# Kernel tuning notes

Measured on AMD Instinct MI355X. Metric: run time of the kernel, lower is better.

## Reference

```python
import math
import jax, jax.numpy as jnp
import numpy as np

EMBED_DIM = 2048
NUM_HEADS = 16
HEAD_DIM = EMBED_DIM // NUM_HEADS
CHUNK = 128
RMS_EPS = 1e-5


def _build_slopes(n):
    # ALiBi-style slopes (power-of-2 branch; n=16 is a power of 2)
    def pow2(n):
        start = 2.0 ** (-(2.0 ** -(math.log2(n) - 3)))
        return [start * (start ** i) for i in range(n)]
    if math.log2(n).is_integer():
        s = pow2(n)
    else:
        closest = 2 ** math.floor(math.log2(n))
        s = pow2(closest) + pow2(2 * closest)[0::2][: n - closest]
    return jnp.asarray(s, dtype=jnp.float32)


def _rotary(x_BTHD, offset=0):
    # x: [B, T, H, D]; D//4 nonzero freqs + D//4 zero freqs -> D//2 angles
    T, D = x_BTHD.shape[1], x_BTHD.shape[-1]
    freq = (1.0 / 1024.0) ** jnp.linspace(0.0, 1.0, D // 4, dtype=jnp.float32)
    freq = jnp.concatenate([freq, jnp.zeros(D // 4, dtype=jnp.float32)])
    t = jnp.arange(offset, offset + T, dtype=jnp.float32)
    theta = t[:, None] * freq[None, :]            # [T, D/2]
    cos = jnp.cos(theta)[None, :, None, :]
    sin = jnp.sin(theta)[None, :, None, :]
    x1, x2 = jnp.split(x_BTHD.astype(jnp.float32), 2, axis=-1)
    y1 = x1 * cos + x2 * sin
    y2 = -x1 * sin + x2 * cos
    return jnp.concatenate([y1, y2], axis=-1).astype(x_BTHD.dtype)


def _lightning_attn(q, k, v, slopes):
    # q,k,v: [B, H, T, D]; decayed causal linear attention:
    #   o_t = q_t @ sum_{s<=t} exp(-slope*(t-s)) * k_s v_s^T
    B, H, T, D = q.shape
    C = CHUNK
    NC = T // C
    r = jnp.exp(-slopes)                          # [H]
    i = jnp.arange(C, dtype=jnp.float32)
    # factors within a chunk
    q_decay = r[:, None] ** (i[None, :] + 1.0)    # [H, C] : r^{i+1}
    k_decay = r[:, None] ** (C - 1.0 - i[None, :])  # [H, C] : r^{C-1-i}
    diff = i[:, None] - i[None, :]                # t - s
    mask = diff >= 0
    dmask = jnp.where(mask[None], r[:, None, None] ** jnp.where(mask, diff, 0.0)[None], 0.0)  # [H,C,C]
    r_C = r ** float(C)                            # [H]

    def reshape_chunks(x):
        return x.reshape(B, H, NC, C, D).transpose(2, 0, 1, 3, 4)  # [NC,B,H,C,D]

    qc, kc, vc = reshape_chunks(q), reshape_chunks(k), reshape_chunks(v)

    def step(kv, qkv):
        qi, ki, vi = qkv                          # [B,H,C,D]
        inter = jnp.einsum('bhcd,bhde->bhce', qi * q_decay[None, :, :, None], kv)
        scores = jnp.einsum('bhcd,bhsd->bhcs', qi, ki) * dmask[None]
        intra = jnp.einsum('bhcs,bhse->bhce', scores, vi)
        kv_new = r_C[None, :, None, None] * kv + jnp.einsum(
            'bhcd,bhce->bhde', ki * k_decay[None, :, :, None], vi)
        return kv_new, inter + intra

    kv0 = jnp.zeros((B, H, D, D), dtype=q.dtype)
    _, out = jax.lax.scan(step, kv0, (qc, kc, vc))  # [NC,B,H,C,D]
    return out.transpose(1, 2, 0, 3, 4).reshape(B, H, T, D)


def _rms_norm(x, w):
    var = jnp.mean(jnp.square(x), axis=-1, keepdims=True)
    return x * jax.lax.rsqrt(var + RMS_EPS) * w


def setup_inputs() -> dict:
    key = jax.random.key(0)
    ks = jax.random.split(key, 6)
    sc = 1.0 / math.sqrt(EMBED_DIM)
    return {
        'x': jax.random.normal(ks[0], (4, 4096, EMBED_DIM), dtype=jnp.float32),
        'Wq': jax.random.normal(ks[1], (EMBED_DIM, EMBED_DIM), dtype=jnp.float32) * sc,
        'Wk': jax.random.normal(ks[2], (EMBED_DIM, EMBED_DIM), dtype=jnp.float32) * sc,
        'Wv': jax.random.normal(ks[3], (EMBED_DIM, EMBED_DIM), dtype=jnp.float32) * sc,
        'Wo': jax.random.normal(ks[4], (EMBED_DIM, EMBED_DIM), dtype=jnp.float32) * sc,
        'rms_w': jnp.ones((EMBED_DIM,), dtype=jnp.float32),
    }


def reference(x, Wq, Wk, Wv, Wo, rms_w):
    B, T, E = x.shape
    H, D = NUM_HEADS, HEAD_DIM
    q = (x @ Wq).reshape(B, T, H, D)
    k = (x @ Wk).reshape(B, T, H, D)
    v = (x @ Wv).reshape(B, T, H, D)
    q = _rotary(q)
    k = _rotary(k)
    q, k, v = (t.transpose(0, 2, 1, 3) for t in (q, k, v))  # [B,H,T,D]
    slopes = _build_slopes(H)
    attn = _lightning_attn(q, k, v, slopes)       # [B,H,T,D]
    attn = attn.transpose(0, 2, 1, 3).reshape(B, T, E)
    attn = _rms_norm(attn, rms_w)
    return attn @ Wo
```

## Files before the change

kernel.cpp:

```cpp
#include <hip/hip_runtime.h>

typedef unsigned short ushort;
typedef float f32x4 __attribute__((ext_vector_type(4)));
typedef __bf16 bf16x8 __attribute__((ext_vector_type(8)));
typedef ushort u16x4 __attribute__((ext_vector_type(4)));
typedef ushort u16x8 __attribute__((ext_vector_type(8)));

#define LOG2E 1.4426950408889634f

__device__ __forceinline__ ushort f2bu(float f) { __bf16 b = (__bf16)f; return __builtin_bit_cast(ushort, b); }
__device__ __forceinline__ float  bu2f(ushort u) { return (float)__builtin_bit_cast(__bf16, u); }

__device__ __forceinline__ void gld16(const void* g, void* l) {
    __builtin_amdgcn_global_load_lds((const __attribute__((address_space(1))) unsigned int*)g,
                                     (__attribute__((address_space(3))) unsigned int*)l, 16, 0, 0);
}

__global__ __launch_bounds__(256) void k_cvt(const float* __restrict__ in, ushort* __restrict__ out, int n4) {
    int i = blockIdx.x * 256 + threadIdx.x;
    if (i < n4) {
        float4 v = ((const float4*)in)[i];
        u16x4 o = { f2bu(v.x), f2bu(v.y), f2bu(v.z), f2bu(v.w) };
        ((u16x4*)out)[i] = o;
    }
}

__global__ __launch_bounds__(256) void k_twt4(const float* __restrict__ W0, const float* __restrict__ W1,
                                              const float* __restrict__ W2, const float* __restrict__ W3,
                                              ushort* __restrict__ D0, ushort* __restrict__ D1,
                                              ushort* __restrict__ D2, ushort* __restrict__ D3) {
    int z = blockIdx.z;
    const float* W = (z == 0) ? W0 : (z == 1) ? W1 : (z == 2) ? W2 : W3;
    ushort* Wt = (z == 0) ? D0 : (z == 1) ? D1 : (z == 2) ? D2 : D3;
    __shared__ float t[32][33];
    int n0 = blockIdx.x * 32, k0 = blockIdx.y * 32;
    int tx = threadIdx.x & 31, ty = threadIdx.x >> 5;
#pragma unroll
    for (int i = 0; i < 32; i += 8) t[ty + i][tx] = W[(size_t)(k0 + ty + i) * 2048 + n0 + tx];
    __syncthreads();
#pragma unroll
    for (int i = 0; i < 32; i += 8) Wt[(size_t)(n0 + ty + i) * 2048 + k0 + tx] = f2bu(t[tx][ty + i]);
}

__global__ __launch_bounds__(256) void k_rope(float* __restrict__ tab) {
    int idx = blockIdx.x * 256 + threadIdx.x;
    int t = idx >> 5, j = idx & 31;
    float fr = exp2f(-10.0f * (float)j / 31.0f);
    float th = (float)t * fr;
    tab[idx * 2]     = cosf(th);
    tab[idx * 2 + 1] = sinf(th);
}

#define AOFF(buf, kh) ((buf) * 32768 + (kh) * 16384)
#define BOFF(buf, kh) (65536 + (buf) * 32768 + (kh) * 16384)

#define STG_A(BUFX, KHX, KKX) do {                                                 \
    gld16(asrc0 + ((KKX) + (KHX) * 32) * 2, lds + AOFF(BUFX, KHX) + ldst);         \
    gld16(asrc1 + ((KKX) + (KHX) * 32) * 2, lds + AOFF(BUFX, KHX) + 8192 + ldst);  \
} while (0)
#define STG_B(BUFX, KHX, KKX) do {                                                 \
    gld16(bsrc0 + ((KKX) + (KHX) * 32) * 2, lds + BOFF(BUFX, KHX) + ldst);         \
    gld16(bsrc1 + ((KKX) + (KHX) * 32) * 2, lds + BOFF(BUFX, KHX) + 8192 + ldst);  \
} while (0)

#define PHASE(BUF, KH, MH, LDB, STAGE_STMT, TAILVM) do {                           \
    bf16x8 af_[4];                                                                 \
    const char* ab_ = lds + AOFF(BUF, KH);                                         \
    _Pragma("unroll")                                                              \
    for (int mi_ = 0; mi_ < 4; ++mi_)                                              \
        af_[mi_] = *(const bf16x8*)(ab_ + offA[(MH) * 4 + mi_]);                   \
    if (LDB) {                                                                     \
        const char* bb_ = lds + BOFF(BUF, KH);                                     \
        _Pragma("unroll")                                                          \
        for (int ni_ = 0; ni_ < 4; ++ni_)                                          \
            bfr[ni_] = *(const bf16x8*)(bb_ + offB[ni_]);                          \
    }                                                                              \
    STAGE_STMT;                                                                    \
    __builtin_amdgcn_s_barrier();                                                  \
    asm volatile("s_waitcnt lgkmcnt(0)" ::: "memory");                             \
    __builtin_amdgcn_sched_barrier(0);                                             \
    __builtin_amdgcn_s_setprio(1);                                                 \
    _Pragma("unroll")                                                              \
    for (int mi_ = 0; mi_ < 4; ++mi_)                                              \
        _Pragma("unroll")                                                          \
        for (int ni_ = 0; ni_ < 4; ++ni_)                                          \
            acc[(MH) * 4 + mi_][ni_] = __builtin_amdgcn_mfma_f32_16x16x32_bf16(    \
                af_[mi_], bfr[ni_], acc[(MH) * 4 + mi_][ni_], 0, 0, 0);            \
    __builtin_amdgcn_s_setprio(0);                                                 \
    TAILVM;                                                                        \
    __builtin_amdgcn_s_barrier();                                                  \
} while (0)

#define TILE(BUF, TC) do {                                                         \
    int tp1_ = (TC) + 1 < 32 ? (TC) + 1 : 31;                                      \
    int tp2_ = (TC) + 2 < 32 ? (TC) + 2 : 31;                                      \
    int kb1_ = tp1_ * 64, kb2_ = tp2_ * 64;                                        \
    PHASE(BUF, 0, 0, 1, STG_A((BUF) ^ 1, 1, kb1_), ((void)0));                     \
    PHASE(BUF, 0, 1, 0, STG_B((BUF) ^ 1, 1, kb1_),                                 \
          asm volatile("s_waitcnt vmcnt(8)" ::: "memory"));                        \
    PHASE(BUF, 1, 0, 1, STG_A(BUF, 0, kb2_), ((void)0));                           \
    PHASE(BUF, 1, 1, 0, STG_B(BUF, 0, kb2_),                                       \
          asm volatile("s_waitcnt vmcnt(8)" ::: "memory"));                        \
} while (0)

template <int MODE>
__global__ __launch_bounds__(512, 2) void k_gemm(const ushort* __restrict__ A, const ushort* __restrict__ Bt,
                                                 const float* __restrict__ rt, float* __restrict__ Cf,
                                                 ushort* __restrict__ qa, ushort* __restrict__ ka,
                                                 ushort* __restrict__ kTa, ushort* __restrict__ vTa) {
    __shared__ __align__(128) char lds[131072];
    const int tid = threadIdx.x;
    const int wid = tid >> 6, lane = tid & 63;
    const int wm = wid >> 2, wn = wid & 3;
    const int lrow = lane & 15, q = lane >> 4;

    int bid = blockIdx.x;
    int xcd = bid & 7, local = bid >> 3;
    int nt, mloc;
    if (MODE == 0) { nt = xcd + (local % 3) * 8; mloc = local / 3; }
    else           { nt = local & 7;             mloc = xcd * 8 + (local >> 3); }
    const size_t n0 = (size_t)nt * 256;
    const size_t m0 = (size_t)mloc * 256;

    int offA[8], offB[4];
#pragma unroll
    for (int mi = 0; mi < 8; ++mi) {
        int R = wm * 128 + mi * 16 + lrow;
        offA[mi] = R * 64 + ((q ^ ((R >> 1) & 3)) << 4);
    }
#pragma unroll
    for (int ni = 0; ni < 4; ++ni) {
        int R = wn * 64 + ni * 16 + lrow;
        offB[ni] = R * 64 + ((q ^ ((R >> 1) & 3)) << 4);
    }

    int srow0 = tid >> 2;
    int cw = (tid & 3) ^ ((tid >> 3) & 3);
    const char* asrc0 = (const char*)(A + (m0 + srow0) * 2048 + cw * 8);
    const char* asrc1 = (const char*)(A + (m0 + srow0 + 128) * 2048 + cw * 8);
    const char* bsrc0 = (const char*)(Bt + (n0 + srow0) * 2048 + cw * 8);
    const char* bsrc1 = (const char*)(Bt + (n0 + srow0 + 128) * 2048 + cw * 8);
    const int ldst = tid * 16;

    f32x4 acc[8][4] = {};
    bf16x8 bfr[4];

    STG_A(0, 0, 0); STG_B(0, 0, 0); STG_A(0, 1, 0); STG_B(0, 1, 0);
    STG_A(1, 0, 64); STG_B(1, 0, 64);
    asm volatile("s_waitcnt vmcnt(8)" ::: "memory");
    __builtin_amdgcn_s_barrier();

#pragma unroll 1
    for (int t = 0; t < 32; t += 2) {
        TILE(0, t);
        TILE(1, t + 1);
    }

    if (MODE == 1) {
#pragma unroll
        for (int mi = 0; mi < 8; ++mi)
#pragma unroll
            for (int ni = 0; ni < 4; ++ni)
#pragma unroll
                for (int i = 0; i < 4; ++i) {
                    size_t row = m0 + wm * 128 + mi * 16 + q * 4 + i;
                    size_t col = n0 + wn * 64 + ni * 16 + lrow;
                    Cf[row * 2048 + col] = acc[mi][ni][i];
                }
        return;
    }

    asm volatile("s_waitcnt vmcnt(0)" ::: "memory");
    __syncthreads();
    ushort* lt = (ushort*)lds;
    const int tsel = nt >> 3;
    const int b = (int)(m0 >> 12);
    const int t0base = (int)(m0 & 4095);
    const int hbase = (nt & 7) * 2;

    for (int st = 0; st < 2; ++st) {
        if (wm == st) {
#pragma unroll
            for (int mi = 0; mi < 8; ++mi)
#pragma unroll
                for (int ni = 0; ni < 4; ++ni)
#pragma unroll
                    for (int i = 0; i < 4; ++i)
                        lt[(mi * 16 + q * 4 + i) * 258 + wn * 64 + ni * 16 + lrow] = f2bu(acc[mi][ni][i]);
        }
        __syncthreads();
        const int t0 = t0base + st * 128;
        if (tsel != 2) {
            int cid = tid & 31, rquad = tid >> 5;
            int d0 = cid * 4;
            ushort* dstN = (tsel == 0 ? qa : ka);
#pragma unroll 2
            for (int it = 0; it < 16; ++it) {
                int hl = it >> 3, rr = (it & 7) * 16 + rquad;
                int t = t0 + rr;
                const ushort* src = &lt[rr * 258 + hl * 128];
                ushort o[4];
                if (d0 < 32) {
#pragma unroll
                    for (int j = 0; j < 4; ++j) {
                        int d = d0 + j;
                        float2 cssn = *(const float2*)&rt[(t * 32 + d) * 2];
                        float x1 = bu2f(src[d]), x2 = bu2f(src[d + 64]);
                        o[j] = f2bu(x1 * cssn.x + x2 * cssn.y);
                    }
                } else if (d0 >= 64 && d0 < 96) {
#pragma unroll
                    for (int j = 0; j < 4; ++j) {
                        int d = d0 + j;
                        float2 cssn = *(const float2*)&rt[(t * 32 + (d - 64)) * 2];
                        float x1 = bu2f(src[d - 64]), x2 = bu2f(src[d]);
                        o[j] = f2bu(x2 * cssn.x - x1 * cssn.y);
                    }
                } else {
#pragma unroll
                    for (int j = 0; j < 4; ++j) o[j] = src[d0 + j];
                }
                int bh = b * 16 + hbase + hl;
                u16x4 ov = { o[0], o[1], o[2], o[3] };
                *(u16x4*)(dstN + ((size_t)bh * 4096 + t) * 128 + d0) = ov;
                if (tsel == 1 && (d0 < 32 || (d0 >= 64 && d0 < 96))) {
                    ushort* wb = &lt[rr * 258 + hl * 128 + d0];
                    wb[0] = o[0]; wb[1] = o[1]; wb[2] = o[2]; wb[3] = o[3];
                }
            }
        }
        if (tsel != 0) {
            __syncthreads();
            int sb = tid & 31, dgrp = tid >> 5;
            int s0 = sb * 4;
            ushort* dstT = (tsel == 1 ? kTa : vTa);
#pragma unroll 2
            for (int it = 0; it < 16; ++it) {
                int hl = it >> 3, dd = (it & 7) * 16 + dgrp;
                int bh = b * 16 + hbase + hl;
                float l2r_h = -exp2f(-0.5f * (float)(hbase + hl + 1)) * LOG2E;
                ushort o[4];
#pragma unroll
                for (int j = 0; j < 4; ++j) {
                    int s = s0 + j;
                    float v = bu2f(lt[s * 258 + hl * 128 + dd]);
                    if (tsel == 1) v *= exp2f(l2r_h * (float)(127 - s));
                    o[j] = f2bu(v);
                }
                u16x4 ov = { o[0], o[1], o[2], o[3] };
                *(u16x4*)(dstT + ((size_t)bh * 128 + dd) * 4096 + t0 + s0) = ov;
            }
        }
        __syncthreads();
    }
}

__global__ __launch_bounds__(256) void k_pass1(const ushort* __restrict__ kTa, const ushort* __restrict__ vTa,
                                               float* __restrict__ KVlo, float* __restrict__ KVhi) {
    int blk = blockIdx.x;
    int c = blk & 31, bh = blk >> 5;
    __shared__ __align__(16) ushort lv[128][136];
    __shared__ __align__(16) ushort lk[128][136];
    int tid = threadIdx.x;
#pragma unroll
    for (int i = 0; i < 8; ++i) {
        int idx = i * 256 + tid; int row = idx >> 4, cb = (idx & 15) * 8;
        *(bf16x8*)&lv[row][cb] = *(const bf16x8*)(vTa + ((size_t)bh * 128 + row) * 4096 + c * 128 + cb);
        *(bf16x8*)&lk[row][cb] = *(const bf16x8*)(kTa + ((size_t)bh * 128 + row) * 4096 + c * 128 + cb);
    }
    __syncthreads();
    int wid = tid >> 6, lane = tid & 63, wr = wid >> 1, wc = wid & 1;
    int lrow = lane & 15, lko = (lane >> 4) * 8;
    f32x4 acc[4][4] = {};
#pragma unroll
    for (int ks = 0; ks < 4; ++ks) {
        bf16x8 a[4], bb[4];
#pragma unroll
        for (int mi = 0; mi < 4; ++mi) a[mi] = *(const bf16x8*)&lv[wr * 64 + mi * 16 + lrow][ks * 32 + lko];
#pragma unroll
        for (int ni = 0; ni < 4; ++ni) bb[ni] = *(const bf16x8*)&lk[wc * 64 + ni * 16 + lrow][ks * 32 + lko];
#pragma unroll
        for (int mi = 0; mi < 4; ++mi)
#pragma unroll
            for (int ni = 0; ni < 4; ++ni)
                acc[mi][ni] = __builtin_amdgcn_mfma_f32_16x16x32_bf16(a[mi], bb[ni], acc[mi][ni], 0, 0, 0);
    }
    float* out = (bh < 32) ? (KVlo + (size_t)blk * 16384) : (KVhi + (size_t)(blk - 1024) * 16384);
#pragma unroll
    for (int mi = 0; mi < 4; ++mi)
#pragma unroll
        for (int ni = 0; ni < 4; ++ni)
#pragma unroll
            for (int i = 0; i < 4; ++i)
                out[(wr * 64 + mi * 16 + (lane >> 4) * 4 + i) * 128 + wc * 64 + ni * 16 + lrow] = acc[mi][ni][i];
}

__global__ __launch_bounds__(256) void k_scan(const float* __restrict__ KVlo, const float* __restrict__ KVhi,
                                              ushort* __restrict__ KVbf) {
    int bh = blockIdx.x >> 4, seg = blockIdx.x & 15, h = bh & 15;
    float slope = exp2f(-0.5f * (float)(h + 1));
    float rC = exp2f(-slope * LOG2E * 128.0f);
    int off = seg * 1024 + threadIdx.x * 4;
    const float* base = (bh < 32) ? (KVlo + (size_t)bh * 32 * 16384) : (KVhi + (size_t)(bh - 32) * 32 * 16384);
    f32x4 st = {0.f, 0.f, 0.f, 0.f};
    for (int c = 0; c < 32; ++c) {
        f32x4 v = *(const f32x4*)(base + (size_t)c * 16384 + off);
        u16x4 o = { f2bu(st.x), f2bu(st.y), f2bu(st.z), f2bu(st.w) };
        *(u16x4*)(KVbf + ((size_t)bh * 32 + c) * 16384 + off) = o;
        st = st * rC + v;
    }
}

__global__ __launch_bounds__(512) void k_pass3(const ushort* __restrict__ qa, const ushort* __restrict__ ka,
                                               const ushort* __restrict__ vTa, const ushort* __restrict__ KVbf,
                                               ushort* __restrict__ attn) {
    int blk = blockIdx.x;
    int c = blk & 31, bh = blk >> 5, h = bh & 15;
    __shared__ __align__(16) ushort lq[128][136];
    __shared__ __align__(16) ushort lk[128][136];
    __shared__ __align__(16) ushort lv[128][136];
    int tid = threadIdx.x;
#pragma unroll
    for (int i = 0; i < 4; ++i) {
        int idx = i * 512 + tid; int row = idx >> 4, cb = (idx & 15) * 8;
        *(bf16x8*)&lq[row][cb] = *(const bf16x8*)(qa + ((size_t)bh * 4096 + c * 128 + row) * 128 + cb);
        *(bf16x8*)&lk[row][cb] = *(const bf16x8*)(ka + ((size_t)bh * 4096 + c * 128 + row) * 128 + cb);
        *(bf16x8*)&lv[row][cb] = *(const bf16x8*)(vTa + ((size_t)bh * 128 + row) * 4096 + c * 128 + cb);
    }
    __syncthreads();
    int wid = tid >> 6, lane = tid & 63;
    int wr = wid >> 2, wc = wid & 3;
    int lrow = lane & 15, lko = (lane >> 4) * 8;
    float slope = exp2f(-0.5f * (float)(h + 1));
    float l2r = -slope * LOG2E;

    f32x4 accs[4][2] = {};
#pragma unroll
    for (int kd = 0; kd < 4; ++kd) {
        bf16x8 a[4], bb[2];
#pragma unroll
        for (int mi = 0; mi < 4; ++mi) a[mi] = *(const bf16x8*)&lq[wr * 64 + mi * 16 + lrow][kd * 32 + lko];
#pragma unroll
        for (int ni = 0; ni < 2; ++ni) bb[ni] = *(const bf16x8*)&lk[wc * 32 + ni * 16 + lrow][kd * 32 + lko];
#pragma unroll
        for (int mi = 0; mi < 4; ++mi)
#pragma unroll
            for (int ni = 0; ni < 2; ++ni)
                accs[mi][ni] = __builtin_amdgcn_mfma_f32_16x16x32_bf16(a[mi], bb[ni], accs[mi][ni], 0, 0, 0);
    }
    __syncthreads();

    f32x4 acc[4][2] = {};
#pragma unroll
    for (int kd = 0; kd < 4; ++kd) {
        bf16x8 a[4], bb[2];
#pragma unroll
        for (int mi = 0; mi < 4; ++mi) a[mi] = *(const bf16x8*)&lq[wr * 64 + mi * 16 + lrow][kd * 32 + lko];
#pragma unroll
        for (int ni = 0; ni < 2; ++ni)
            bb[ni] = *(const bf16x8*)(KVbf + (size_t)blk * 16384 + (size_t)(wc * 32 + ni * 16 + lrow) * 128 + kd * 32 + lko);
#pragma unroll
        for (int mi = 0; mi < 4; ++mi)
#pragma unroll
            for (int ni = 0; ni < 2; ++ni)
                acc[mi][ni] = __builtin_amdgcn_mfma_f32_16x16x32_bf16(a[mi], bb[ni], acc[mi][ni], 0, 0, 0);
    }

#pragma unroll
    for (int mi = 0; mi < 4; ++mi)
#pragma unroll
        for (int ni = 0; ni < 2; ++ni)
#pragma unroll
            for (int i = 0; i < 4; ++i) {
                int t = wr * 64 + mi * 16 + (lane >> 4) * 4 + i;
                int s = wc * 32 + ni * 16 + lrow;
                int dt = t - s;
                float w = (dt < 0) ? 0.f : exp2f(l2r * (float)dt);
                lk[t][s] = f2bu(accs[mi][ni][i] * w);
            }

#pragma unroll
    for (int mi = 0; mi < 4; ++mi)
#pragma unroll
        for (int ni = 0; ni < 2; ++ni)
#pragma unroll
            for (int i = 0; i < 4; ++i) {
                int t = wr * 64 + mi * 16 + (lane >> 4) * 4 + i;
                acc[mi][ni][i] *= exp2f(l2r * (float)(t + 1));
            }
    __syncthreads();

#pragma unroll
    for (int ks = 0; ks < 4; ++ks) {
        bf16x8 a[4], bb[2];
#pragma unroll
        for (int mi = 0; mi < 4; ++mi) a[mi] = *(const bf16x8*)&lk[wr * 64 + mi * 16 + lrow][ks * 32 + lko];
#pragma unroll
        for (int ni = 0; ni < 2; ++ni) bb[ni] = *(const bf16x8*)&lv[wc * 32 + ni * 16 + lrow][ks * 32 + lko];
#pragma unroll
        for (int mi = 0; mi < 4; ++mi)
#pragma unroll
            for (int ni = 0; ni < 2; ++ni)
                acc[mi][ni] = __builtin_amdgcn_mfma_f32_16x16x32_bf16(a[mi], bb[ni], acc[mi][ni], 0, 0, 0);
    }

    ushort* out = attn + ((size_t)bh * 4096 + c * 128) * 128;
#pragma unroll
    for (int mi = 0; mi < 4; ++mi)
#pragma unroll
        for (int ni = 0; ni < 2; ++ni)
#pragma unroll
            for (int i = 0; i < 4; ++i)
                out[(size_t)(wr * 64 + mi * 16 + (lane >> 4) * 4 + i) * 128 + wc * 32 + ni * 16 + lrow] =
                    f2bu(acc[mi][ni][i]);
}

__global__ __launch_bounds__(256) void k_rms(const ushort* __restrict__ attn, const float* __restrict__ w,
                                             ushort* __restrict__ normed) {
    int tok = blockIdx.x; int b = tok >> 12, t = tok & 4095;
    int tid = threadIdx.x;
    int e0 = tid * 8; int h = e0 >> 7, d0 = e0 & 127;
    bf16x8 v = *(const bf16x8*)(attn + (((size_t)(b * 16 + h) * 4096 + t) * 128 + d0));
    float f[8]; float ss = 0.f;
#pragma unroll
    for (int j = 0; j < 8; ++j) { f[j] = (float)v[j]; ss += f[j] * f[j]; }
#pragma unroll
    for (int o = 1; o < 64; o <<= 1) ss += __shfl_xor(ss, o, 64);
    __shared__ float red[4];
    if ((tid & 63) == 0) red[tid >> 6] = ss;
    __syncthreads();
    float tot = red[0] + red[1] + red[2] + red[3];
    float sc = rsqrtf(tot * (1.0f / 2048.0f) + 1e-5f);
    u16x8 ov;
#pragma unroll
    for (int j = 0; j < 8; ++j) ov[j] = f2bu(f[j] * sc * w[e0 + j]);
    *(u16x8*)(normed + (size_t)tok * 2048 + e0) = ov;
}

extern "C" void kernel_launch(void* const* d_in, const int* in_sizes, int n_in,
                              void* d_out, int out_size, void* d_ws, size_t ws_size,
                              hipStream_t stream) {
    const float* x    = (const float*)d_in[0];
    const float* Wq   = (const float*)d_in[1];
    const float* Wk   = (const float*)d_in[2];
    const float* Wv   = (const float*)d_in[3];
    const float* Wo   = (const float*)d_in[4];
    const float* rmsw = (const float*)d_in[5];
    char* ws = (char*)d_ws;
    const size_t MiB = 1ull << 20;
    ushort* WtQKV = (ushort*)(ws + 0);
    ushort* WtK   = (ushort*)(ws + 8 * MiB);
    ushort* WtV   = (ushort*)(ws + 16 * MiB);
    ushort* WtO   = (ushort*)(ws + 24 * MiB);
    ushort* xb    = (ushort*)(ws + 32 * MiB);
    ushort* qa    = (ushort*)(ws + 96 * MiB);
    ushort* ka    = (ushort*)(ws + 160 * MiB);
    ushort* kTa   = (ushort*)(ws + 224 * MiB);
    ushort* vTa   = (ushort*)(ws + 288 * MiB);
    float*  rt    = (float*)(ws + 352 * MiB);
    float*  KVlo  = (float*)(ws + 32 * MiB);
    float*  KVhi  = (float*)(ws + 353 * MiB);
    ushort* KVbf  = (ushort*)(ws + 224 * MiB);
    ushort* attn  = (ushort*)(ws + 32 * MiB);
    ushort* nrm   = (ushort*)(ws + 96 * MiB);

    k_cvt<<<32768, 256, 0, stream>>>(x, xb, 8388608);
    dim3 gw(64, 64, 4);
    k_twt4<<<gw, 256, 0, stream>>>(Wq, Wk, Wv, Wo, WtQKV, WtK, WtV, WtO);
    k_rope<<<512, 256, 0, stream>>>(rt);

    k_gemm<0><<<1536, 512, 0, stream>>>(xb, WtQKV, rt, nullptr, qa, ka, kTa, vTa);

    k_pass1<<<2048, 256, 0, stream>>>(kTa, vTa, KVlo, KVhi);
    k_scan<<<1024, 256, 0, stream>>>(KVlo, KVhi, KVbf);
    k_pass3<<<2048, 512, 0, stream>>>(qa, ka, vTa, KVbf, attn);

    k_rms<<<16384, 256, 0, stream>>>(attn, rmsw, nrm);
    k_gemm<1><<<512, 512, 0, stream>>>(nrm, WtO, nullptr, (float*)d_out, nullptr, nullptr, nullptr, nullptr);
}
```

Before: 822.2 us.

## Transpose GEMM epilogue LDS tile and store per-chunk KV states in bf16

The QKV GEMM epilogue now stages its tile in LDS column-major (d-major, pitch 130) with packed 32-bit writes. The rope and transposed-store passes restructure their thread mapping around this layout, writing pairs of elements at a time. Per-chunk KV outer products from pass1 are now stored as bf16 in one contiguous buffer instead of fp32 split across two regions, which halves pass1 write and scan read traffic. The cost is lower precision for the chunk states fed into the scan, and the rope path's LDS reads are now strided, so bank conflicts may change.

```diff
diff --git a/kernel.cpp b/kernel.cpp
--- a/kernel.cpp
+++ b/kernel.cpp
@@ -1,6 +1,7 @@
 #include <hip/hip_runtime.h>
 
 typedef unsigned short ushort;
+typedef unsigned int uint;
 typedef float f32x4 __attribute__((ext_vector_type(4)));
 typedef __bf16 bf16x8 __attribute__((ext_vector_type(8)));
 typedef ushort u16x4 __attribute__((ext_vector_type(4)));
@@ -10,6 +11,7 @@
 
 __device__ __forceinline__ ushort f2bu(float f) { __bf16 b = (__bf16)f; return __builtin_bit_cast(ushort, b); }
 __device__ __forceinline__ float  bu2f(ushort u) { return (float)__builtin_bit_cast(__bf16, u); }
+__device__ __forceinline__ uint   pk2(float a, float b) { return (uint)f2bu(a) | ((uint)f2bu(b) << 16); }
 
 __device__ __forceinline__ void gld16(const void* g, void* l) {
     __builtin_amdgcn_global_load_lds((const __attribute__((address_space(1))) unsigned int*)g,
@@ -183,49 +185,51 @@
 #pragma unroll
             for (int mi = 0; mi < 8; ++mi)
 #pragma unroll
-                for (int ni = 0; ni < 4; ++ni)
-#pragma unroll
-                    for (int i = 0; i < 4; ++i)
-                        lt[(mi * 16 + q * 4 + i) * 258 + wn * 64 + ni * 16 + lrow] = f2bu(acc[mi][ni][i]);
+                for (int ni = 0; ni < 4; ++ni) {
+                    int col = wn * 64 + ni * 16 + lrow;
+                    int r0 = mi * 16 + q * 4;
+                    uint* p = (uint*)&lt[col * 130 + r0];
+                    p[0] = pk2(acc[mi][ni][0], acc[mi][ni][1]);
+                    p[1] = pk2(acc[mi][ni][2], acc[mi][ni][3]);
+                }
         }
         __syncthreads();
         const int t0 = t0base + st * 128;
+
         if (tsel != 2) {
-            int cid = tid & 31, rquad = tid >> 5;
-            int d0 = cid * 4;
+            int cid = tid & 63, rgrp = tid >> 6;
             ushort* dstN = (tsel == 0 ? qa : ka);
 #pragma unroll 2
-            for (int it = 0; it < 16; ++it) {
-                int hl = it >> 3, rr = (it & 7) * 16 + rquad;
-                int t = t0 + rr;
-                const ushort* src = &lt[rr * 258 + hl * 128];
-                ushort o[4];
-                if (d0 < 32) {
-#pragma unroll
-                    for (int j = 0; j < 4; ++j) {
-                        int d = d0 + j;
-                        float2 cssn = *(const float2*)&rt[(t * 32 + d) * 2];
-                        float x1 = bu2f(src[d]), x2 = bu2f(src[d + 64]);
-                        o[j] = f2bu(x1 * cssn.x + x2 * cssn.y);
+            for (int hl = 0; hl < 2; ++hl) {
+                int bh = b * 16 + hbase + hl;
+                size_t rowbase = ((size_t)bh * 4096 + t0) * 128;
+#pragma unroll 4
+                for (int it = 0; it < 16; ++it) {
+                    int rr = it * 8 + rgrp;
+                    int t = t0 + rr;
+                    if (cid < 16) {
+                        int d0 = cid * 2;
+                        float4 cs = *(const float4*)&rt[(t * 32 + d0) * 2];
+                        float xa0 = bu2f(lt[(hl * 128 + d0) * 130 + rr]);
+                        float xa1 = bu2f(lt[(hl * 128 + d0 + 1) * 130 + rr]);
+                        float xb0 = bu2f(lt[(hl * 128 + d0 + 64) * 130 + rr]);
+                        float xb1 = bu2f(lt[(hl * 128 + d0 + 65) * 130 + rr]);
+                        uint y1 = pk2(xa0 * cs.x + xb0 * cs.y, xa1 * cs.z + xb1 * cs.w);
+                        uint y2 = pk2(xb0 * cs.x - xa0 * cs.y, xb1 * cs.z - xa1 * cs.w);
+                        *(uint*)(dstN + rowbase + (size_t)rr * 128 + d0) = y1;
+                        *(uint*)(dstN + rowbase + (size_t)rr * 128 + d0 + 64) = y2;
+                        if (tsel == 1) {
+                            lt[(hl * 128 + d0) * 130 + rr] = (ushort)(y1 & 0xffff);
+                            lt[(hl * 128 + d0 + 1) * 130 + rr] = (ushort)(y1 >> 16);
+                            lt[(hl * 128 + d0 + 64) * 130 + rr] = (ushort)(y2 & 0xffff);
+                            lt[(hl * 128 + d0 + 65) * 130 + rr] = (ushort)(y2 >> 16);
+                        }
+                    } else if (cid < 48) {
+                        int d0 = (cid < 32) ? (2 * cid) : (32 + 2 * cid);
+                        uint v = (uint)lt[(hl * 128 + d0) * 130 + rr] |
+                                 ((uint)lt[(hl * 128 + d0 + 1) * 130 + rr] << 16);
+                        *(uint*)(dstN + rowbase + (size_t)rr * 128 + d0) = v;
                     }
-                } else if (d0 >= 64 && d0 < 96) {
-#pragma unroll
-                    for (int j = 0; j < 4; ++j) {
-                        int d = d0 + j;
-                        float2 cssn = *(const float2*)&rt[(t * 32 + (d - 64)) * 2];
-                        float x1 = bu2f(src[d - 64]), x2 = bu2f(src[d]);
-                        o[j] = f2bu(x2 * cssn.x - x1 * cssn.y);
-                    }
-                } else {
-#pragma unroll
-                    for (int j = 0; j < 4; ++j) o[j] = src[d0 + j];
-                }
-                int bh = b * 16 + hbase + hl;
-                u16x4 ov = { o[0], o[1], o[2], o[3] };
-                *(u16x4*)(dstN + ((size_t)bh * 4096 + t) * 128 + d0) = ov;
-                if (tsel == 1 && (d0 < 32 || (d0 >= 64 && d0 < 96))) {
-                    ushort* wb = &lt[rr * 258 + hl * 128 + d0];
-                    wb[0] = o[0]; wb[1] = o[1]; wb[2] = o[2]; wb[3] = o[3];
                 }
             }
         }
@@ -234,21 +238,27 @@
             int sb = tid & 31, dgrp = tid >> 5;
             int s0 = sb * 4;
             ushort* dstT = (tsel == 1 ? kTa : vTa);
-#pragma unroll 2
-            for (int it = 0; it < 16; ++it) {
-                int hl = it >> 3, dd = (it & 7) * 16 + dgrp;
+            for (int hl = 0; hl < 2; ++hl) {
                 int bh = b * 16 + hbase + hl;
                 float l2r_h = -exp2f(-0.5f * (float)(hbase + hl + 1)) * LOG2E;
-                ushort o[4];
-#pragma unroll
-                for (int j = 0; j < 4; ++j) {
-                    int s = s0 + j;
-                    float v = bu2f(lt[s * 258 + hl * 128 + dd]);
-                    if (tsel == 1) v *= exp2f(l2r_h * (float)(127 - s));
-                    o[j] = f2bu(v);
+#pragma unroll 2
+                for (int itg = 0; itg < 8; ++itg) {
+                    int dd = itg * 16 + dgrp;
+                    const uint* p = (const uint*)&lt[(hl * 128 + dd) * 130 + s0];
+                    uint w0 = p[0], w1 = p[1];
+                    u16x4 ov;
+                    if (tsel == 1) {
+                        float v0 = bu2f((ushort)(w0 & 0xffff)) * exp2f(l2r_h * (float)(127 - s0));
+                        float v1 = bu2f((ushort)(w0 >> 16))    * exp2f(l2r_h * (float)(126 - s0));
+                        float v2 = bu2f((ushort)(w1 & 0xffff)) * exp2f(l2r_h * (float)(125 - s0));
+                        float v3 = bu2f((ushort)(w1 >> 16))    * exp2f(l2r_h * (float)(124 - s0));
+                        ov[0] = f2bu(v0); ov[1] = f2bu(v1); ov[2] = f2bu(v2); ov[3] = f2bu(v3);
+                    } else {
+                        ov[0] = (ushort)(w0 & 0xffff); ov[1] = (ushort)(w0 >> 16);
+                        ov[2] = (ushort)(w1 & 0xffff); ov[3] = (ushort)(w1 >> 16);
+                    }
+                    *(u16x4*)(dstT + ((size_t)bh * 128 + dd) * 4096 + t0 + s0) = ov;
                 }
-                u16x4 ov = { o[0], o[1], o[2], o[3] };
-                *(u16x4*)(dstT + ((size_t)bh * 128 + dd) * 4096 + t0 + s0) = ov;
             }
         }
         __syncthreads();
@@ -256,7 +266,7 @@
 }
 
 __global__ __launch_bounds__(256) void k_pass1(const ushort* __restrict__ kTa, const ushort* __restrict__ vTa,
-                                               float* __restrict__ KVlo, float* __restrict__ KVhi) {
+                                               ushort* __restrict__ KVc) {
     int blk = blockIdx.x;
     int c = blk & 31, bh = blk >> 5;
     __shared__ __align__(16) ushort lv[128][136];
@@ -285,29 +295,31 @@
             for (int ni = 0; ni < 4; ++ni)
                 acc[mi][ni] = __builtin_amdgcn_mfma_f32_16x16x32_bf16(a[mi], bb[ni], acc[mi][ni], 0, 0, 0);
     }
-    float* out = (bh < 32) ? (KVlo + (size_t)blk * 16384) : (KVhi + (size_t)(blk - 1024) * 16384);
+    ushort* out = KVc + (size_t)blk * 16384;
 #pragma unroll
     for (int mi = 0; mi < 4; ++mi)
 #pragma unroll
         for (int ni = 0; ni < 4; ++ni)
 #pragma unroll
             for (int i = 0; i < 4; ++i)
-                out[(wr * 64 + mi * 16 + (lane >> 4) * 4 + i) * 128 + wc * 64 + ni * 16 + lrow] = acc[mi][ni][i];
-}
-
-__global__ __launch_bounds__(256) void k_scan(const float* __restrict__ KVlo, const float* __restrict__ KVhi,
-                                              ushort* __restrict__ KVbf) {
+                out[(wr * 64 + mi * 16 + (lane >> 4) * 4 + i) * 128 + wc * 64 + ni * 16 + lrow] = f2bu(acc[mi][ni][i]);
+}
+
+__global__ __launch_bounds__(256) void k_scan(const ushort* __restrict__ KVc, ushort* __restrict__ KVbf) {
     int bh = blockIdx.x >> 4, seg = blockIdx.x & 15, h = bh & 15;
     float slope = exp2f(-0.5f * (float)(h + 1));
     float rC = exp2f(-slope * LOG2E * 128.0f);
     int off = seg * 1024 + threadIdx.x * 4;
-    const float* base = (bh < 32) ? (KVlo + (size_t)bh * 32 * 16384) : (KVhi + (size_t)(bh - 32) * 32 * 16384);
     f32x4 st = {0.f, 0.f, 0.f, 0.f};
     for (int c = 0; c < 32; ++c) {
-        f32x4 v = *(const f32x4*)(base + (size_t)c * 16384 + off);
+        size_t base = ((size_t)bh * 32 + c) * 16384 + off;
+        u16x4 vb = *(const u16x4*)(KVc + base);
         u16x4 o = { f2bu(st.x), f2bu(st.y), f2bu(st.z), f2bu(st.w) };
-        *(u16x4*)(KVbf + ((size_t)bh * 32 + c) * 16384 + off) = o;
-        st = st * rC + v;
+        *(u16x4*)(KVbf + base) = o;
+        st.x = st.x * rC + bu2f(vb[0]);
+        st.y = st.y * rC + bu2f(vb[1]);
+        st.z = st.z * rC + bu2f(vb[2]);
+        st.w = st.w * rC + bu2f(vb[3]);
     }
 }
 
@@ -458,8 +470,7 @@
     ushort* kTa   = (ushort*)(ws + 224 * MiB);
     ushort* vTa   = (ushort*)(ws + 288 * MiB);
     float*  rt    = (float*)(ws + 352 * MiB);
-    float*  KVlo  = (float*)(ws + 32 * MiB);
-    float*  KVhi  = (float*)(ws + 353 * MiB);
+    ushort* KVc   = (ushort*)(ws + 353 * MiB);
     ushort* KVbf  = (ushort*)(ws + 224 * MiB);
     ushort* attn  = (ushort*)(ws + 32 * MiB);
     ushort* nrm   = (ushort*)(ws + 96 * MiB);
@@ -471,8 +482,8 @@
 
     k_gemm<0><<<1536, 512, 0, stream>>>(xb, WtQKV, rt, nullptr, qa, ka, kTa, vTa);
 
-    k_pass1<<<2048, 256, 0, stream>>>(kTa, vTa, KVlo, KVhi);
-    k_scan<<<1024, 256, 0, stream>>>(KVlo, KVhi, KVbf);
+    k_pass1<<<2048, 256, 0, stream>>>(kTa, vTa, KVc);
+    k_scan<<<1024, 256, 0, stream>>>(KVc, KVbf);
     k_pass3<<<2048, 512, 0, stream>>>(qa, ka, vTa, KVbf, attn);
 
     k_rms<<<16384, 256, 0, stream>>>(attn, rmsw, nrm);
```

After: 820.4 us. No clear change (-0.2%).
